# Kernel tuning notes

Hardware: AMD Instinct MI355X
Metric: run time of the kernel (lower is better)

## Reference

```python
import jax, jax.numpy as jnp
import numpy as np

N = 50000
E = 400000
IN_DIM = 16
EMB = 32
HID = 128
HEADS = 4
LAYERS = 3
EPS_BN = 1e-5
NEG_SLOPE = 0.2


def setup_inputs() -> dict:
    key = jax.random.key(0)
    ks = jax.random.split(key, 16)
    s = 0.1
    C = HID  # per-head out channels (concat=False)
    inp = {
        "x": jax.random.normal(ks[0], (N, IN_DIM), jnp.float32),
        "edge_index": jax.random.randint(ks[1], (2, E), 0, N, jnp.int64),
        "emb": s * jax.random.normal(ks[2], (N, EMB), jnp.float32),
        "Wf": s * jax.random.normal(ks[3], (EMB, IN_DIM), jnp.float32),
        "bf": jnp.zeros((EMB,), jnp.float32),
        "Wc": s * jax.random.normal(ks[4], (HID, 2 * EMB), jnp.float32),
        "bc": jnp.zeros((HID,), jnp.float32),
        "Wl": s * jax.random.normal(ks[5], (LAYERS, HEADS * C, HID), jnp.float32),
        "a_src": s * jax.random.normal(ks[6], (LAYERS, HEADS, C), jnp.float32),
        "a_dst": s * jax.random.normal(ks[7], (LAYERS, HEADS, C), jnp.float32),
        "bl": jnp.zeros((LAYERS, C), jnp.float32),
        "gamma": jnp.ones((LAYERS, C), jnp.float32),
        "beta": jnp.zeros((LAYERS, C), jnp.float32),
        "Wout": s * jax.random.normal(ks[8], (1, HID), jnp.float32),
        "bout": jnp.zeros((1,), jnp.float32),
    }
    return inp


def _gat_layer(h, src, dst, W, a_s, a_d, b):
    n = h.shape[0]
    C = W.shape[0] // HEADS
    hp = (h @ W.T).reshape(n, HEADS, C)                # (N,H,C)
    al_s = jnp.sum(hp * a_s, axis=-1)                  # (N,H)
    al_d = jnp.sum(hp * a_d, axis=-1)                  # (N,H)
    e = jax.nn.leaky_relu(al_s[src] + al_d[dst], NEG_SLOPE)  # (E,H)
    m = jax.ops.segment_max(e, dst, num_segments=n)    # per-target max
    ex = jnp.exp(e - m[dst])
    denom = jax.ops.segment_sum(ex, dst, num_segments=n) + 1e-16
    alpha = ex / denom[dst]                            # (E,H)
    msg = hp[src] * alpha[..., None]                   # (E,H,C)
    out = jax.ops.segment_sum(msg, dst, num_segments=n)
    return jnp.mean(out, axis=1) + b                   # concat=False: head mean


def _bn(x, g, b):
    mu = jnp.mean(x, axis=0)
    var = jnp.var(x, axis=0)  # biased, as torch BN uses for normalization
    return (x - mu) * jax.lax.rsqrt(var + EPS_BN) * g + b


def reference(x, edge_index, emb, Wf, bf, Wc, bc, Wl, a_src, a_dst, bl, gamma, beta, Wout, bout):
    n = x.shape[0]
    loop = jnp.arange(n, dtype=edge_index.dtype)
    src = jnp.concatenate([edge_index[0], loop])       # add self loops
    dst = jnp.concatenate([edge_index[1], loop])
    feat = x @ Wf.T + bf
    h = jax.nn.relu(jnp.concatenate([emb, feat], axis=1) @ Wc.T + bc)
    prev_h = h
    for i in range(LAYERS):
        h = _gat_layer(h, src, dst, Wl[i], a_src[i], a_dst[i], bl[i])
        h = jax.nn.relu(_bn(h, gamma[i], beta[i]))
        if prev_h.shape == h.shape:
            h = h + prev_h
        prev_h = h
    out = h @ Wout.T + bout
    return jnp.clip(out, -10.0, 10.0)
```

## Files before the change

kernel.cpp:

```cpp
#include <hip/hip_runtime.h>
#include <hip/hip_bf16.h>
#include <math.h>

#define INDIM 16
#define EMBD 32
#define UDIM 64
#define HIDD 128
#define HEADS 4
#define LAYERS 3
#define MPAD 50048
#define NSLICE 32

typedef short v8s __attribute__((ext_vector_type(8)));
typedef float v4f __attribute__((ext_vector_type(4)));

__device__ __forceinline__ float lrelu(float x) { return x > 0.f ? x : 0.2f * x; }
__device__ __forceinline__ float bf2f(unsigned int bits16) {
    unsigned int u = bits16 << 16;
    return __builtin_bit_cast(float, u);
}
__device__ __forceinline__ unsigned short f2bf(float f) {
    unsigned int u = __builtin_bit_cast(unsigned int, f);
    unsigned int lsb = (u >> 16) & 1;
    u += 0x7fff + lsb;
    return (unsigned short)(u >> 16);
}

__global__ __launch_bounds__(256) void k_enc(const float* __restrict__ x,
                                             const float* __restrict__ emb,
                                             const float* __restrict__ Wf,
                                             const float* __restrict__ bf,
                                             unsigned short* __restrict__ u, int n) {
    int i = blockIdx.x * 256 + threadIdx.x;
    if (i >= n * EMBD) return;
    int node = i >> 5, j = i & 31;
    const float* xr = x + (size_t)node * INDIM;
    const float* wr = Wf + (size_t)j * INDIM;
    float s = bf[j];
#pragma unroll
    for (int k = 0; k < INDIM; k++) s += xr[k] * wr[k];
    u[(size_t)node * UDIM + EMBD + j] = f2bf(s);
    u[(size_t)node * UDIM + j] = f2bf(emb[(size_t)node * EMBD + j]);
}

__global__ __launch_bounds__(256) void k_prep_v(const float* __restrict__ Wl,
                                                unsigned short* __restrict__ Vb) {
    int i = blockIdx.x * 256 + threadIdx.x;
    if (i >= LAYERS * HIDD * 512) return;
    int l = i >> 16;
    int rem = i & 65535;
    int c = rem >> 9;
    int f = rem & 511;
    int h = f >> 7, k = f & 127;
    Vb[i] = f2bf(Wl[(size_t)l * 512 * HIDD + (size_t)(h * HIDD + c) * HIDD + k]);
}

__global__ __launch_bounds__(256) void k_prep_a(const float* __restrict__ Wl,
                                                const float* __restrict__ a_s,
                                                const float* __restrict__ a_d,
                                                float* __restrict__ ws, float* __restrict__ wd) {
    int i = blockIdx.x * 256 + threadIdx.x;
    if (i >= LAYERS * HEADS * HIDD) return;
    int l = i >> 9, h = (i >> 7) & 3, k = i & 127;
    const float* W = Wl + (size_t)l * 512 * HIDD;
    const float* as = a_s + l * 512 + h * HIDD;
    const float* ad = a_d + l * 512 + h * HIDD;
    float ss = 0.f, sd = 0.f;
    for (int c = 0; c < HIDD; c++) {
        float w = W[(size_t)(h * HIDD + c) * HIDD + k];
        ss += as[c] * w;
        sd += ad[c] * w;
    }
    ws[i] = ss;
    wd[i] = sd;
}

__global__ __launch_bounds__(256) void k_prep_wc(const float* __restrict__ Wc,
                                                 unsigned short* __restrict__ Wcb) {
    int i = blockIdx.x * 256 + threadIdx.x;
    if (i < HIDD * UDIM) Wcb[i] = f2bf(Wc[i]);
}

__global__ __launch_bounds__(256) void k_gemm_enc(const unsigned short* __restrict__ A,
                                                  const unsigned short* __restrict__ B,
                                                  const float* __restrict__ bias,
                                                  float* __restrict__ O,
                                                  unsigned short* __restrict__ Ob, int M) {
    const int K = UDIM;
    int tid = threadIdx.x;
    int lane = tid & 63, wid = tid >> 6;
    int wm = wid >> 1, wn = wid & 1;
    int bm = blockIdx.x * 128;
    int lr = lane & 15, lk = lane >> 4;
    v4f acc[4][4] = {};
    const unsigned short* Abase = A + (size_t)(bm + wm * 64 + lr) * K + lk * 8;
    const unsigned short* Bbase = B + (size_t)(wn * 64 + lr) * K + lk * 8;
#pragma unroll
    for (int kk = 0; kk < K / 32; kk++) {
        v8s a[4], b[4];
#pragma unroll
        for (int f = 0; f < 4; f++) {
            a[f] = *(const v8s*)(Abase + (size_t)(f * 16) * K + kk * 32);
            b[f] = *(const v8s*)(Bbase + (size_t)(f * 16) * K + kk * 32);
        }
#pragma unroll
        for (int i = 0; i < 4; i++)
#pragma unroll
            for (int j = 0; j < 4; j++)
                acc[i][j] = __builtin_amdgcn_mfma_f32_16x16x32_bf16(a[i], b[j], acc[i][j], 0, 0, 0);
    }
#pragma unroll
    for (int i = 0; i < 4; i++) {
#pragma unroll
        for (int r = 0; r < 4; r++) {
            int row = bm + wm * 64 + i * 16 + lk * 4 + r;
            if (row >= M) continue;
#pragma unroll
            for (int j = 0; j < 4; j++) {
                int col = wn * 64 + j * 16 + lr;
                float v = fmaxf(acc[i][j][r] + bias[col], 0.f);
                O[(size_t)row * HIDD + col] = v;
                Ob[(size_t)row * HIDD + col] = f2bf(v);
            }
        }
    }
}

__global__ __launch_bounds__(256) void k_deg(const int* __restrict__ ei, int* __restrict__ deg,
                                             int E, int tot) {
    int e = blockIdx.x * 256 + threadIdx.x;
    if (e >= tot) return;
    int dst = (e < E) ? ei[E + e] : (e - E);
    atomicAdd(&deg[dst], 1);
}

__global__ __launch_bounds__(256) void k_scan1(const int* __restrict__ deg,
                                               int* __restrict__ rowptr,
                                               int* __restrict__ partials, int n) {
    int tid = threadIdx.x;
    int i = blockIdx.x * 256 + tid;
    int v = (i < n) ? deg[i] : 0;
    __shared__ int sm[256];
    sm[tid] = v;
    __syncthreads();
    for (int off = 1; off < 256; off <<= 1) {
        int t = (tid >= off) ? sm[tid - off] : 0;
        __syncthreads();
        sm[tid] += t;
        __syncthreads();
    }
    if (i < n) rowptr[i] = sm[tid] - v;
    if (tid == 255) partials[blockIdx.x] = sm[255];
}

__global__ __launch_bounds__(256) void k_scan2(int* __restrict__ partials, int nb) {
    int tid = threadIdx.x;
    int v = (tid < nb) ? partials[tid] : 0;
    __shared__ int sm[256];
    sm[tid] = v;
    __syncthreads();
    for (int off = 1; off < 256; off <<= 1) {
        int t = (tid >= off) ? sm[tid - off] : 0;
        __syncthreads();
        sm[tid] += t;
        __syncthreads();
    }
    if (tid < nb) partials[tid] = sm[tid] - v;
}

__global__ __launch_bounds__(256) void k_scan3(const int* __restrict__ deg,
                                               const int* __restrict__ partials,
                                               int* __restrict__ rowptr,
                                               int* __restrict__ cursor, int n) {
    int i = blockIdx.x * 256 + threadIdx.x;
    if (i >= n) return;
    int r = rowptr[i] + partials[blockIdx.x];
    rowptr[i] = r;
    cursor[i] = r;
    if (i == n - 1) rowptr[n] = r + deg[i];
}

__global__ __launch_bounds__(256) void k_scatter(const int* __restrict__ ei, int* __restrict__ cursor,
                                                 int* __restrict__ csr_src, int E, int tot) {
    int e = blockIdx.x * 256 + threadIdx.x;
    if (e >= tot) return;
    int src = (e < E) ? ei[e] : (e - E);
    int dst = (e < E) ? ei[E + e] : (e - E);
    int pos = atomicAdd(&cursor[dst], 1);
    csr_src[pos] = src;
}

__global__ __launch_bounds__(256) void k_al0(const float* __restrict__ h,
                                             const float* __restrict__ ws,
                                             const float* __restrict__ wd,
                                             float* __restrict__ al_s, float* __restrict__ al_d,
                                             int n) {
    int wid = threadIdx.x >> 6, lane = threadIdx.x & 63;
    int node = blockIdx.x * 4 + wid;
    if (node >= n) return;
    float2 v = *(const float2*)(h + (size_t)node * HIDD + 2 * lane);
    float s[8];
#pragma unroll
    for (int hh = 0; hh < 4; hh++) {
        float2 w1 = *(const float2*)(ws + hh * HIDD + 2 * lane);
        float2 w2 = *(const float2*)(wd + hh * HIDD + 2 * lane);
        s[hh] = v.x * w1.x + v.y * w1.y;
        s[4 + hh] = v.x * w2.x + v.y * w2.y;
    }
#pragma unroll
    for (int o = 32; o; o >>= 1)
#pragma unroll
        for (int q = 0; q < 8; q++) s[q] += __shfl_xor(s[q], o);
    if (lane == 0) {
        *(float4*)(al_s + (size_t)node * 4) = make_float4(s[0], s[1], s[2], s[3]);
        *(float4*)(al_d + (size_t)node * 4) = make_float4(s[4], s[5], s[6], s[7]);
    }
}

__global__ __launch_bounds__(1024) void k_layer(const int* __restrict__ rowptr,
                                                const int* __restrict__ csr_src,
                                                const float* __restrict__ al_s,
                                                const float* __restrict__ al_d,
                                                const unsigned short* __restrict__ hb,
                                                const unsigned short* __restrict__ Vb,
                                                float* __restrict__ agg,
                                                float* __restrict__ bns, int n) {
    __shared__ unsigned int Gw[16 * 256];
    __shared__ float s1[128], s2[128];
    __shared__ int Ssrc[16][64];
    __shared__ float Sal[16][4][64];
    int tid = threadIdx.x, lane = tid & 63, w = tid >> 6;
    if (tid < 128) { s1[tid] = 0.f; s2[tid] = 0.f; }
    int node0 = blockIdx.x * 16;
    int node = node0 + w;
    const float4* als4 = (const float4*)al_s;
    const unsigned int* h2 = (const unsigned int*)hb;
    int sw = (w & 7) << 2;

    if (node < n) {
        int start = rowptr[node], end = rowptr[node + 1];
        int deg = end - start;
        float4 ad = ((const float4*)al_d)[node];
        if (deg <= 64) {
            bool act = lane < deg;
            int src_l = act ? csr_src[start + lane] : 0;
            float e0 = -3.0e38f, e1 = -3.0e38f, e2 = -3.0e38f, e3 = -3.0e38f;
            if (act) {
                float4 as = als4[src_l];
                e0 = lrelu(as.x + ad.x);
                e1 = lrelu(as.y + ad.y);
                e2 = lrelu(as.z + ad.z);
                e3 = lrelu(as.w + ad.w);
            }
            int span = 1;
            while (span < deg) span <<= 1;
            float m0 = e0, m1 = e1, m2 = e2, m3 = e3;
            for (int o = 1; o < span; o <<= 1) {
                m0 = fmaxf(m0, __shfl_xor(m0, o));
                m1 = fmaxf(m1, __shfl_xor(m1, o));
                m2 = fmaxf(m2, __shfl_xor(m2, o));
                m3 = fmaxf(m3, __shfl_xor(m3, o));
            }
            float p0 = act ? expf(e0 - m0) : 0.f;
            float p1 = act ? expf(e1 - m1) : 0.f;
            float p2 = act ? expf(e2 - m2) : 0.f;
            float p3 = act ? expf(e3 - m3) : 0.f;
            float t0 = p0, t1 = p1, t2 = p2, t3 = p3;
            for (int o = 1; o < span; o <<= 1) {
                t0 += __shfl_xor(t0, o);
                t1 += __shfl_xor(t1, o);
                t2 += __shfl_xor(t2, o);
                t3 += __shfl_xor(t3, o);
            }
            Ssrc[w][lane] = src_l;
            Sal[w][0][lane] = p0 / (t0 + 1e-16f);
            Sal[w][1][lane] = p1 / (t1 + 1e-16f);
            Sal[w][2][lane] = p2 / (t2 + 1e-16f);
            Sal[w][3][lane] = p3 / (t3 + 1e-16f);

            float acc[4][2] = {};
            for (int j0 = 0; j0 < deg; j0 += 4) {
                int4 s4 = *(const int4*)&Ssrc[w][j0];
                float4 af0 = *(const float4*)&Sal[w][0][j0];
                float4 af1 = *(const float4*)&Sal[w][1][j0];
                float4 af2 = *(const float4*)&Sal[w][2][j0];
                float4 af3 = *(const float4*)&Sal[w][3][j0];
                unsigned int u0 = h2[(size_t)s4.x * 64 + lane];
                unsigned int u1 = h2[(size_t)s4.y * 64 + lane];
                unsigned int u2 = h2[(size_t)s4.z * 64 + lane];
                unsigned int u3 = h2[(size_t)s4.w * 64 + lane];
                float x0, x1;
                x0 = bf2f(u0 & 0xffff); x1 = bf2f(u0 >> 16);
                acc[0][0] += af0.x * x0; acc[0][1] += af0.x * x1;
                acc[1][0] += af1.x * x0; acc[1][1] += af1.x * x1;
                acc[2][0] += af2.x * x0; acc[2][1] += af2.x * x1;
                acc[3][0] += af3.x * x0; acc[3][1] += af3.x * x1;
                x0 = bf2f(u1 & 0xffff); x1 = bf2f(u1 >> 16);
                acc[0][0] += af0.y * x0; acc[0][1] += af0.y * x1;
                acc[1][0] += af1.y * x0; acc[1][1] += af1.y * x1;
                acc[2][0] += af2.y * x0; acc[2][1] += af2.y * x1;
                acc[3][0] += af3.y * x0; acc[3][1] += af3.y * x1;
                x0 = bf2f(u2 & 0xffff); x1 = bf2f(u2 >> 16);
                acc[0][0] += af0.z * x0; acc[0][1] += af0.z * x1;
                acc[1][0] += af1.z * x0; acc[1][1] += af1.z * x1;
                acc[2][0] += af2.z * x0; acc[2][1] += af2.z * x1;
                acc[3][0] += af3.z * x0; acc[3][1] += af3.z * x1;
                x0 = bf2f(u3 & 0xffff); x1 = bf2f(u3 >> 16);
                acc[0][0] += af0.w * x0; acc[0][1] += af0.w * x1;
                acc[1][0] += af1.w * x0; acc[1][1] += af1.w * x1;
                acc[2][0] += af2.w * x0; acc[2][1] += af2.w * x1;
                acc[3][0] += af3.w * x0; acc[3][1] += af3.w * x1;
            }
#pragma unroll
            for (int hh = 0; hh < 4; hh++) {
                unsigned int p = (unsigned int)f2bf(acc[hh][0]) |
                                 ((unsigned int)f2bf(acc[hh][1]) << 16);
                Gw[w * 256 + ((hh * 64 + lane) ^ sw)] = p;
            }
        } else {
            float m0 = -3.0e38f, m1 = -3.0e38f, m2 = -3.0e38f, m3 = -3.0e38f;
            for (int j = start + lane; j < end; j += 64) {
                float4 as = als4[csr_src[j]];
                m0 = fmaxf(m0, lrelu(as.x + ad.x));
                m1 = fmaxf(m1, lrelu(as.y + ad.y));
                m2 = fmaxf(m2, lrelu(as.z + ad.z));
                m3 = fmaxf(m3, lrelu(as.w + ad.w));
            }
#pragma unroll
            for (int o = 32; o; o >>= 1) {
                m0 = fmaxf(m0, __shfl_xor(m0, o));
                m1 = fmaxf(m1, __shfl_xor(m1, o));
                m2 = fmaxf(m2, __shfl_xor(m2, o));
                m3 = fmaxf(m3, __shfl_xor(m3, o));
            }
            float t0 = 0.f, t1 = 0.f, t2 = 0.f, t3 = 0.f;
            for (int j = start + lane; j < end; j += 64) {
                float4 as = als4[csr_src[j]];
                t0 += expf(lrelu(as.x + ad.x) - m0);
                t1 += expf(lrelu(as.y + ad.y) - m1);
                t2 += expf(lrelu(as.z + ad.z) - m2);
                t3 += expf(lrelu(as.w + ad.w) - m3);
            }
#pragma unroll
            for (int o = 32; o; o >>= 1) {
                t0 += __shfl_xor(t0, o);
                t1 += __shfl_xor(t1, o);
                t2 += __shfl_xor(t2, o);
                t3 += __shfl_xor(t3, o);
            }
            float i0 = 1.f / (t0 + 1e-16f), i1 = 1.f / (t1 + 1e-16f);
            float i2 = 1.f / (t2 + 1e-16f), i3 = 1.f / (t3 + 1e-16f);
            float acc[4][2] = {};
            for (int base = start; base < end; base += 64) {
                int cnt = min(64, end - base);
                bool act2 = lane < cnt;
                int src_l = act2 ? csr_src[base + lane] : 0;
                float a0 = 0.f, a1 = 0.f, a2 = 0.f, a3 = 0.f;
                if (act2) {
                    float4 as = als4[src_l];
                    a0 = expf(lrelu(as.x + ad.x) - m0) * i0;
                    a1 = expf(lrelu(as.y + ad.y) - m1) * i1;
                    a2 = expf(lrelu(as.z + ad.z) - m2) * i2;
                    a3 = expf(lrelu(as.w + ad.w) - m3) * i3;
                }
                for (int jj = 0; jj < cnt; jj++) {
                    int sj = __shfl(src_l, jj);
                    float b0 = __shfl(a0, jj), b1 = __shfl(a1, jj);
                    float b2 = __shfl(a2, jj), b3 = __shfl(a3, jj);
                    unsigned int uu = h2[(size_t)sj * 64 + lane];
                    float x0 = bf2f(uu & 0xffff), x1 = bf2f(uu >> 16);
                    acc[0][0] += b0 * x0; acc[0][1] += b0 * x1;
                    acc[1][0] += b1 * x0; acc[1][1] += b1 * x1;
                    acc[2][0] += b2 * x0; acc[2][1] += b2 * x1;
                    acc[3][0] += b3 * x0; acc[3][1] += b3 * x1;
                }
            }
#pragma unroll
            for (int hh = 0; hh < 4; hh++) {
                unsigned int p = (unsigned int)f2bf(acc[hh][0]) |
                                 ((unsigned int)f2bf(acc[hh][1]) << 16);
                Gw[w * 256 + ((hh * 64 + lane) ^ sw)] = p;
            }
        }
    } else {
#pragma unroll
        for (int hh = 0; hh < 4; hh++) Gw[w * 256 + ((hh * 64 + lane) ^ sw)] = 0;
    }
    __syncthreads();

    if (w < 8) {
        int lr = lane & 15, lk = lane >> 4;
        int swr = (lr & 7) << 2;
        v4f a2 = {};
        const unsigned short* Bb = Vb + (size_t)(w * 16 + lr) * 512 + lk * 8;
#pragma unroll
        for (int kk = 0; kk < 16; kk++) {
            v8s a = *(const v8s*)(&Gw[lr * 256 + ((kk * 16 + lk * 4) ^ swr)]);
            v8s b = *(const v8s*)(Bb + kk * 32);
            a2 = __builtin_amdgcn_mfma_f32_16x16x32_bf16(a, b, a2, 0, 0, 0);
        }
        int col = w * 16 + lr;
        float ls = 0.f, lq = 0.f;
#pragma unroll
        for (int r = 0; r < 4; r++) {
            int nd = node0 + lk * 4 + r;
            float v = a2[r];
            if (nd < n) {
                agg[(size_t)nd * HIDD + col] = v;
                ls += v;
                lq += v * v;
            }
        }
        atomicAdd(&s1[col], ls);
        atomicAdd(&s2[col], lq);
    }
    __syncthreads();
    if (tid < 128) {
        float* slice = bns + (size_t)(blockIdx.x & (NSLICE - 1)) * 256;
        atomicAdd(&slice[tid], s1[tid]);
        atomicAdd(&slice[128 + tid], s2[tid]);
    }
}

__global__ __launch_bounds__(128) void k_bnfin(const float* __restrict__ bns,
                                               const float* __restrict__ gamma,
                                               const float* __restrict__ beta,
                                               float* __restrict__ scale,
                                               float* __restrict__ shift, float invn) {
    int c = threadIdx.x;
    float s = 0.f, q = 0.f;
    for (int sl = 0; sl < NSLICE; sl++) {
        s += bns[sl * 256 + c];
        q += bns[sl * 256 + 128 + c];
    }
    float mu = s * invn;
    float var = q * invn - mu * mu;
    float sc = gamma[c] * rsqrtf(0.0625f * var + 1e-5f) * 0.25f;
    scale[c] = sc;
    shift[c] = beta[c] - mu * sc;
}

template <int MODE>
__global__ __launch_bounds__(256) void k_apply(const float* __restrict__ agg,
                                               const float* __restrict__ scale,
                                               const float* __restrict__ shift,
                                               float* __restrict__ h,
                                               unsigned short* __restrict__ hb,
                                               const float* __restrict__ ws,
                                               const float* __restrict__ wd,
                                               float* __restrict__ al_s,
                                               float* __restrict__ al_d,
                                               const float* __restrict__ Wout,
                                               const float* __restrict__ bout,
                                               float* __restrict__ out, int n) {
    int wid = threadIdx.x >> 6, lane = threadIdx.x & 63;
    int node = blockIdx.x * 4 + wid;
    if (node >= n) return;
    int c0 = 2 * lane, c1 = 2 * lane + 1;
    float2 ag = *(const float2*)(agg + (size_t)node * HIDD + c0);
    float2 ho = *(const float2*)(h + (size_t)node * HIDD + c0);
    float v0 = fmaxf(ag.x * scale[c0] + shift[c0], 0.f) + ho.x;
    float v1 = fmaxf(ag.y * scale[c1] + shift[c1], 0.f) + ho.y;
    if (MODE == 0) {
        *(float2*)(h + (size_t)node * HIDD + c0) = make_float2(v0, v1);
        ((unsigned int*)hb)[(size_t)node * 64 + lane] =
            (unsigned int)f2bf(v0) | ((unsigned int)f2bf(v1) << 16);
        float s[8];
#pragma unroll
        for (int hh = 0; hh < 4; hh++) {
            float2 w1 = *(const float2*)(ws + hh * HIDD + c0);
            float2 w2 = *(const float2*)(wd + hh * HIDD + c0);
            s[hh] = v0 * w1.x + v1 * w1.y;
            s[4 + hh] = v0 * w2.x + v1 * w2.y;
        }
#pragma unroll
        for (int o = 32; o; o >>= 1)
#pragma unroll
            for (int q = 0; q < 8; q++) s[q] += __shfl_xor(s[q], o);
        if (lane == 0) {
            *(float4*)(al_s + (size_t)node * 4) = make_float4(s[0], s[1], s[2], s[3]);
            *(float4*)(al_d + (size_t)node * 4) = make_float4(s[4], s[5], s[6], s[7]);
        }
    } else {
        float2 w = *(const float2*)(Wout + c0);
        float p = v0 * w.x + v1 * w.y;
#pragma unroll
        for (int o = 32; o; o >>= 1) p += __shfl_xor(p, o);
        if (lane == 0) {
            float v = p + bout[0];
            out[node] = fminf(fmaxf(v, -10.f), 10.f);
        }
    }
}

extern "C" void kernel_launch(void* const* d_in, const int* in_sizes, int n_in,
                              void* d_out, int out_size, void* d_ws, size_t ws_size,
                              hipStream_t stream) {
    const float* x = (const float*)d_in[0];
    const int* ei = (const int*)d_in[1];
    const float* emb = (const float*)d_in[2];
    const float* Wf = (const float*)d_in[3];
    const float* bf = (const float*)d_in[4];
    const float* Wc = (const float*)d_in[5];
    const float* bc = (const float*)d_in[6];
    const float* Wl = (const float*)d_in[7];
    const float* a_src = (const float*)d_in[8];
    const float* a_dst = (const float*)d_in[9];
    const float* gamma = (const float*)d_in[11];
    const float* beta = (const float*)d_in[12];
    const float* Wout = (const float*)d_in[13];
    const float* bout = (const float*)d_in[14];
    float* out = (float*)d_out;

    int n = in_sizes[0] / INDIM;
    int E = in_sizes[1] / 2;
    int tot = E + n;
    int NB = (n + 255) / 256;

    size_t off = 0;
    auto alloc = [&](size_t bytes) {
        void* p = (char*)d_ws + off;
        off = (off + bytes + 255) & ~(size_t)255;
        return p;
    };
    unsigned short* u = (unsigned short*)alloc((size_t)MPAD * UDIM * 2);
    float* h = (float*)alloc((size_t)MPAD * HIDD * 4);
    unsigned short* hb = (unsigned short*)alloc((size_t)MPAD * HIDD * 2);
    float* agg = (float*)alloc((size_t)MPAD * HIDD * 4);
    float* al_s = (float*)alloc((size_t)n * HEADS * 4);
    float* al_d = (float*)alloc((size_t)n * HEADS * 4);
    int* deg = (int*)alloc((size_t)n * 4);
    int* rowptr = (int*)alloc(((size_t)n + 1) * 4);
    int* cursor = (int*)alloc((size_t)n * 4);
    int* csr_src = (int*)alloc((size_t)tot * 4);
    int* partials = (int*)alloc((size_t)NB * 4);
    unsigned short* Vb = (unsigned short*)alloc((size_t)LAYERS * HIDD * 512 * 2);
    unsigned short* Wcb = (unsigned short*)alloc((size_t)HIDD * UDIM * 2);
    float* ws = (float*)alloc((size_t)LAYERS * HEADS * HIDD * 4);
    float* wd = (float*)alloc((size_t)LAYERS * HEADS * HIDD * 4);
    float* bnsums = (float*)alloc((size_t)LAYERS * NSLICE * 256 * 4);
    float* scale = (float*)alloc(128 * 4);
    float* shift = (float*)alloc(128 * 4);
    (void)ws_size;

    hipMemsetAsync(deg, 0, (size_t)n * 4, stream);
    hipMemsetAsync(bnsums, 0, (size_t)LAYERS * NSLICE * 256 * 4, stream);
    if (n < MPAD) {
        hipMemsetAsync(u + (size_t)n * UDIM, 0, (size_t)(MPAD - n) * UDIM * 2, stream);
    }

    k_prep_v<<<(LAYERS * HIDD * 512 + 255) / 256, 256, 0, stream>>>(Wl, Vb);
    k_prep_a<<<(LAYERS * HEADS * HIDD + 255) / 256, 256, 0, stream>>>(Wl, a_src, a_dst, ws, wd);
    k_prep_wc<<<(HIDD * UDIM + 255) / 256, 256, 0, stream>>>(Wc, Wcb);

    k_deg<<<(tot + 255) / 256, 256, 0, stream>>>(ei, deg, E, tot);
    k_scan1<<<NB, 256, 0, stream>>>(deg, rowptr, partials, n);
    k_scan2<<<1, 256, 0, stream>>>(partials, NB);
    k_scan3<<<NB, 256, 0, stream>>>(deg, partials, rowptr, cursor, n);
    k_scatter<<<(tot + 255) / 256, 256, 0, stream>>>(ei, cursor, csr_src, E, tot);

    k_enc<<<(n * EMBD + 255) / 256, 256, 0, stream>>>(x, emb, Wf, bf, u, n);
    k_gemm_enc<<<MPAD / 128, 256, 0, stream>>>(u, Wcb, bc, h, hb, n);
    k_al0<<<(n + 3) / 4, 256, 0, stream>>>(h, ws, wd, al_s, al_d, n);

    float invn = 1.0f / (float)n;
    int NLB = (n + 15) / 16;
    for (int l = 0; l < LAYERS; l++) {
        k_layer<<<NLB, 1024, 0, stream>>>(rowptr, csr_src, al_s, al_d, hb,
                                          Vb + (size_t)l * HIDD * 512, agg,
                                          bnsums + (size_t)l * NSLICE * 256, n);
        k_bnfin<<<1, 128, 0, stream>>>(bnsums + (size_t)l * NSLICE * 256, gamma + l * HIDD,
                                       beta + l * HIDD, scale, shift, invn);
        if (l < LAYERS - 1)
            k_apply<0><<<(n + 3) / 4, 256, 0, stream>>>(
                agg, scale, shift, h, hb,
                ws + (size_t)(l + 1) * 512, wd + (size_t)(l + 1) * 512, al_s, al_d,
                nullptr, nullptr, nullptr, n);
        else
            k_apply<1><<<(n + 3) / 4, 256, 0, stream>>>(
                agg, scale, shift, h, hb,
                nullptr, nullptr, nullptr, nullptr, Wout, bout, out, n);
    }
}
```

Measured before the change: 464.7 us.

## Shrink GAT layer blocks to 4 nodes and fold BN finalize into apply

The layer kernel now uses 256-thread blocks covering 4 nodes instead of 1024-thread blocks covering 16. The MFMA projection is restructured so each of the 4 waves computes 32 output columns, with the 16-row A tile padded by clamping rows beyond 4 to a zero row. The separate single-block BN finalize kernel is removed, and every apply thread recomputes scale and shift from the slice sums. This aims for better occupancy and one fewer launch per layer. The cost is 12 of 16 MFMA rows doing wasted work, more per-block atomics to the BN slices, and redundant reduction reads in apply.

```diff
diff --git a/kernel.cpp b/kernel.cpp
--- a/kernel.cpp
+++ b/kernel.cpp
@@ -217,25 +217,26 @@
     }
 }
 
-__global__ __launch_bounds__(1024) void k_layer(const int* __restrict__ rowptr,
-                                                const int* __restrict__ csr_src,
-                                                const float* __restrict__ al_s,
-                                                const float* __restrict__ al_d,
-                                                const unsigned short* __restrict__ hb,
-                                                const unsigned short* __restrict__ Vb,
-                                                float* __restrict__ agg,
-                                                float* __restrict__ bns, int n) {
-    __shared__ unsigned int Gw[16 * 256];
+__global__ __launch_bounds__(256) void k_layer(const int* __restrict__ rowptr,
+                                               const int* __restrict__ csr_src,
+                                               const float* __restrict__ al_s,
+                                               const float* __restrict__ al_d,
+                                               const unsigned short* __restrict__ hb,
+                                               const unsigned short* __restrict__ Vb,
+                                               float* __restrict__ agg,
+                                               float* __restrict__ bns, int n) {
+    __shared__ unsigned int Gw[5 * 256];
     __shared__ float s1[128], s2[128];
-    __shared__ int Ssrc[16][64];
-    __shared__ float Sal[16][4][64];
+    __shared__ int Ssrc[4][64];
+    __shared__ float Sal[4][4][64];
     int tid = threadIdx.x, lane = tid & 63, w = tid >> 6;
     if (tid < 128) { s1[tid] = 0.f; s2[tid] = 0.f; }
-    int node0 = blockIdx.x * 16;
+    Gw[4 * 256 + tid] = 0;
+    int node0 = blockIdx.x * 4;
     int node = node0 + w;
     const float4* als4 = (const float4*)al_s;
     const unsigned int* h2 = (const unsigned int*)hb;
-    int sw = (w & 7) << 2;
+    int sw = w << 2;
 
     if (node < n) {
         int start = rowptr[node], end = rowptr[node + 1];
@@ -388,31 +389,41 @@
     }
     __syncthreads();
 
-    if (w < 8) {
+    {
         int lr = lane & 15, lk = lane >> 4;
-        int swr = (lr & 7) << 2;
-        v4f a2 = {};
-        const unsigned short* Bb = Vb + (size_t)(w * 16 + lr) * 512 + lk * 8;
+        int rmin = min(lr, 4);
+        int swr = (rmin & 3) << 2;
+        const unsigned int* Arow = &Gw[rmin * 256];
+        v4f a2[2] = {{}, {}};
+        const unsigned short* Bb0 = Vb + (size_t)(w * 32 + lr) * 512 + lk * 8;
+        const unsigned short* Bb1 = Bb0 + (size_t)16 * 512;
 #pragma unroll
         for (int kk = 0; kk < 16; kk++) {
-            v8s a = *(const v8s*)(&Gw[lr * 256 + ((kk * 16 + lk * 4) ^ swr)]);
-            v8s b = *(const v8s*)(Bb + kk * 32);
-            a2 = __builtin_amdgcn_mfma_f32_16x16x32_bf16(a, b, a2, 0, 0, 0);
-        }
-        int col = w * 16 + lr;
-        float ls = 0.f, lq = 0.f;
-#pragma unroll
-        for (int r = 0; r < 4; r++) {
-            int nd = node0 + lk * 4 + r;
-            float v = a2[r];
-            if (nd < n) {
-                agg[(size_t)nd * HIDD + col] = v;
-                ls += v;
-                lq += v * v;
-            }
-        }
-        atomicAdd(&s1[col], ls);
-        atomicAdd(&s2[col], lq);
+            v8s a = *(const v8s*)(&Arow[(kk * 16 + lk * 4) ^ swr]);
+            v8s b0 = *(const v8s*)(Bb0 + kk * 32);
+            v8s b1 = *(const v8s*)(Bb1 + kk * 32);
+            a2[0] = __builtin_amdgcn_mfma_f32_16x16x32_bf16(a, b0, a2[0], 0, 0, 0);
+            a2[1] = __builtin_amdgcn_mfma_f32_16x16x32_bf16(a, b1, a2[1], 0, 0, 0);
+        }
+        if (lk == 0) {
+#pragma unroll
+            for (int j = 0; j < 2; j++) {
+                int col = w * 32 + j * 16 + lr;
+                float ls = 0.f, lq = 0.f;
+#pragma unroll
+                for (int r = 0; r < 4; r++) {
+                    int nd = node0 + r;
+                    float v = a2[j][r];
+                    if (nd < n) {
+                        agg[(size_t)nd * HIDD + col] = v;
+                        ls += v;
+                        lq += v * v;
+                    }
+                }
+                atomicAdd(&s1[col], ls);
+                atomicAdd(&s2[col], lq);
+            }
+        }
     }
     __syncthreads();
     if (tid < 128) {
@@ -422,28 +433,11 @@
     }
 }
 
-__global__ __launch_bounds__(128) void k_bnfin(const float* __restrict__ bns,
+template <int MODE>
+__global__ __launch_bounds__(256) void k_apply(const float* __restrict__ agg,
+                                               const float* __restrict__ bns,
                                                const float* __restrict__ gamma,
                                                const float* __restrict__ beta,
-                                               float* __restrict__ scale,
-                                               float* __restrict__ shift, float invn) {
-    int c = threadIdx.x;
-    float s = 0.f, q = 0.f;
-    for (int sl = 0; sl < NSLICE; sl++) {
-        s += bns[sl * 256 + c];
-        q += bns[sl * 256 + 128 + c];
-    }
-    float mu = s * invn;
-    float var = q * invn - mu * mu;
-    float sc = gamma[c] * rsqrtf(0.0625f * var + 1e-5f) * 0.25f;
-    scale[c] = sc;
-    shift[c] = beta[c] - mu * sc;
-}
-
-template <int MODE>
-__global__ __launch_bounds__(256) void k_apply(const float* __restrict__ agg,
-                                               const float* __restrict__ scale,
-                                               const float* __restrict__ shift,
                                                float* __restrict__ h,
                                                unsigned short* __restrict__ hb,
                                                const float* __restrict__ ws,
@@ -452,15 +446,31 @@
                                                float* __restrict__ al_d,
                                                const float* __restrict__ Wout,
                                                const float* __restrict__ bout,
-                                               float* __restrict__ out, int n) {
+                                               float* __restrict__ out,
+                                               float invn, int n) {
     int wid = threadIdx.x >> 6, lane = threadIdx.x & 63;
     int node = blockIdx.x * 4 + wid;
     if (node >= n) return;
     int c0 = 2 * lane, c1 = 2 * lane + 1;
+    float s0 = 0.f, q0 = 0.f, s1v = 0.f, q1v = 0.f;
+    for (int sl = 0; sl < NSLICE; sl++) {
+        float2 a = *(const float2*)(bns + sl * 256 + c0);
+        float2 b = *(const float2*)(bns + sl * 256 + 128 + c0);
+        s0 += a.x; s1v += a.y;
+        q0 += b.x; q1v += b.y;
+    }
+    float mu0 = s0 * invn, mu1 = s1v * invn;
+    float va0 = q0 * invn - mu0 * mu0;
+    float va1 = q1v * invn - mu1 * mu1;
+    float sc0 = gamma[c0] * rsqrtf(0.0625f * va0 + 1e-5f) * 0.25f;
+    float sc1 = gamma[c1] * rsqrtf(0.0625f * va1 + 1e-5f) * 0.25f;
+    float sh0 = beta[c0] - mu0 * sc0;
+    float sh1 = beta[c1] - mu1 * sc1;
+
     float2 ag = *(const float2*)(agg + (size_t)node * HIDD + c0);
     float2 ho = *(const float2*)(h + (size_t)node * HIDD + c0);
-    float v0 = fmaxf(ag.x * scale[c0] + shift[c0], 0.f) + ho.x;
-    float v1 = fmaxf(ag.y * scale[c1] + shift[c1], 0.f) + ho.y;
+    float v0 = fmaxf(ag.x * sc0 + sh0, 0.f) + ho.x;
+    float v1 = fmaxf(ag.y * sc1 + sh1, 0.f) + ho.y;
     if (MODE == 0) {
         *(float2*)(h + (size_t)node * HIDD + c0) = make_float2(v0, v1);
         ((unsigned int*)hb)[(size_t)node * 64 + lane] =
@@ -539,8 +549,6 @@
     float* ws = (float*)alloc((size_t)LAYERS * HEADS * HIDD * 4);
     float* wd = (float*)alloc((size_t)LAYERS * HEADS * HIDD * 4);
     float* bnsums = (float*)alloc((size_t)LAYERS * NSLICE * 256 * 4);
-    float* scale = (float*)alloc(128 * 4);
-    float* shift = (float*)alloc(128 * 4);
     (void)ws_size;
 
     hipMemsetAsync(deg, 0, (size_t)n * 4, stream);
@@ -564,21 +572,19 @@
     k_al0<<<(n + 3) / 4, 256, 0, stream>>>(h, ws, wd, al_s, al_d, n);
 
     float invn = 1.0f / (float)n;
-    int NLB = (n + 15) / 16;
+    int NLB = (n + 3) / 4;
     for (int l = 0; l < LAYERS; l++) {
-        k_layer<<<NLB, 1024, 0, stream>>>(rowptr, csr_src, al_s, al_d, hb,
-                                          Vb + (size_t)l * HIDD * 512, agg,
-                                          bnsums + (size_t)l * NSLICE * 256, n);
-        k_bnfin<<<1, 128, 0, stream>>>(bnsums + (size_t)l * NSLICE * 256, gamma + l * HIDD,
-                                       beta + l * HIDD, scale, shift, invn);
+        k_layer<<<NLB, 256, 0, stream>>>(rowptr, csr_src, al_s, al_d, hb,
+                                         Vb + (size_t)l * HIDD * 512, agg,
+                                         bnsums + (size_t)l * NSLICE * 256, n);
         if (l < LAYERS - 1)
             k_apply<0><<<(n + 3) / 4, 256, 0, stream>>>(
-                agg, scale, shift, h, hb,
-                ws + (size_t)(l + 1) * 512, wd + (size_t)(l + 1) * 512, al_s, al_d,
-                nullptr, nullptr, nullptr, n);
+                agg, bnsums + (size_t)l * NSLICE * 256, gamma + l * HIDD, beta + l * HIDD,
+                h, hb, ws + (size_t)(l + 1) * 512, wd + (size_t)(l + 1) * 512, al_s, al_d,
+                nullptr, nullptr, nullptr, invn, n);
         else
             k_apply<1><<<(n + 3) / 4, 256, 0, stream>>>(
-                agg, scale, shift, h, hb,
-                nullptr, nullptr, nullptr, nullptr, Wout, bout, out, n);
-    }
-}
+                agg, bnsums + (size_t)l * NSLICE * 256, gamma + l * HIDD, beta + l * HIDD,
+                h, hb, nullptr, nullptr, nullptr, nullptr, Wout, bout, out, invn, n);
+    }
+}
```

Measured after the change: 1.016 ms. 119% more time.
